# Optimization experiments

Measured on AMD Instinct MI355X. Metric: run time of the kernel, lower is better.

Reference implementation:

```python
import jax, jax.numpy as jnp
import numpy as np

E, H = 1024, 16
N, S, T = 2, 2048, 2048


def setup_inputs() -> dict:
    key = jax.random.key(0)
    ks = jax.random.split(key, 8)
    scale = 1.0 / np.sqrt(E)
    q = jax.random.normal(ks[0], (N, S, E), dtype=jnp.float32)
    k = jax.random.normal(ks[1], (N, T, E), dtype=jnp.float32)
    v = jax.random.normal(ks[2], (N, T, E), dtype=jnp.float32)
    pad_mask = jax.random.randint(ks[3], (N, 1, 1, T), 0, 2, dtype=jnp.int32)
    subsq_mask = jnp.tril(jnp.ones((S, T), dtype=jnp.int32))[None, None]
    Wq = jax.random.normal(ks[4], (E, E), dtype=jnp.float32) * scale
    Wk = jax.random.normal(ks[5], (E, E), dtype=jnp.float32) * scale
    Wv = jax.random.normal(ks[6], (E, E), dtype=jnp.float32) * scale
    bq = jnp.zeros((E,), dtype=jnp.float32)
    bk = jnp.zeros((E,), dtype=jnp.float32)
    bv = jnp.zeros((E,), dtype=jnp.float32)
    return {"query": q, "key": k, "value": v, "pad_mask": pad_mask,
            "subsq_mask": subsq_mask, "Wq": Wq, "bq": bq, "Wk": Wk,
            "bk": bk, "Wv": Wv, "bv": bv}


def reference(query, key, value, pad_mask, subsq_mask, Wq, bq, Wk, bk, Wv, bv):
    n, s, e = query.shape
    t = value.shape[1]
    d = e // H
    # Linear projections (torch Linear: x @ W^T + b), split into heads
    q = (query @ Wq.T + bq).reshape(n, s, H, d).transpose(0, 2, 1, 3)  # [N,H,S,D]
    k = (key @ Wk.T + bk).reshape(n, t, H, d).transpose(0, 2, 1, 3)    # [N,H,T,D]
    v = (value @ Wv.T + bv).reshape(n, t, H, d).transpose(0, 2, 1, 3)  # [N,H,T,D]
    att = jnp.einsum('bhsd,bhtd->bhst', q, k) / jnp.sqrt(jnp.float32(d))
    att = jnp.where(pad_mask == 0, jnp.float32(-1e9), att)
    att = jnp.where(subsq_mask == 0, jnp.float32(-1e9), att)
    prob = jax.nn.softmax(att, axis=-1)
    out = jnp.einsum('bhst,bhtd->bhsd', prob, v)  # [N,H,S,D]
    return out.transpose(0, 2, 1, 3).reshape(n, s, e)
```

## Files before the change

kernel.cpp:

```cpp
#include <hip/hip_runtime.h>

#define HEADS 16
#define DH    64
#define EMB   1024
#define NBAT  2
#define SEQ   2048
#define KDIM  1024
#define NROW  (NBAT * SEQ)

typedef __attribute__((ext_vector_type(8))) short short8;
typedef __attribute__((ext_vector_type(4))) short short4v;
typedef __attribute__((ext_vector_type(4))) float floatx4;
typedef unsigned short u16;
typedef unsigned int   u32;
typedef unsigned long long u64;

__device__ __forceinline__ u16 f2bf(float x) {
    u32 u = __builtin_bit_cast(u32, x);
    u += 0x7fffu + ((u >> 16) & 1u);
    return (u16)(u >> 16);
}
__device__ __forceinline__ float bf2f(u16 v) {
    return __builtin_bit_cast(float, ((u32)v) << 16);
}

__device__ __forceinline__ void gll16(const u16* g, u16* l) {
    __builtin_amdgcn_global_load_lds((const __attribute__((address_space(1))) u32*)g,
                                     (__attribute__((address_space(3))) u32*)l, 16, 0, 0);
}

__global__ __launch_bounds__(256) void cvt_kernel(
    const float* __restrict__ q, const float* __restrict__ k, const float* __restrict__ v,
    const float* __restrict__ wq, const float* __restrict__ wk, const float* __restrict__ wv,
    u16* __restrict__ xb, u16* __restrict__ wb)
{
    const int z = blockIdx.y;
    const float* src; u16* dst; int n;
    if (z < 3) { src = (z == 0) ? q : (z == 1) ? k : v;     dst = xb + (size_t)z * 4194304;       n = 4194304; }
    else       { src = (z == 3) ? wq : (z == 4) ? wk : wv;  dst = wb + (size_t)(z - 3) * 1048576; n = 1048576; }
    for (int i = (blockIdx.x * 256 + threadIdx.x) * 8; i < n; i += 512 * 256 * 8) {
        float4 a = *(const float4*)(src + i);
        float4 b = *(const float4*)(src + i + 4);
        short8 o;
        o[0] = (short)f2bf(a.x); o[1] = (short)f2bf(a.y); o[2] = (short)f2bf(a.z); o[3] = (short)f2bf(a.w);
        o[4] = (short)f2bf(b.x); o[5] = (short)f2bf(b.y); o[6] = (short)f2bf(b.z); o[7] = (short)f2bf(b.w);
        *(short8*)(dst + i) = o;
    }
}

__global__ __launch_bounds__(256) void proj_kernel(
    const u16* __restrict__ xb, const u16* __restrict__ wb,
    const float* __restrict__ bq, const float* __restrict__ bk, const float* __restrict__ bv,
    u16* __restrict__ qh, u16* __restrict__ kh, u16* __restrict__ vt)
{
    const int f = blockIdx.x;
    const int xcd = f & 7, jj = f >> 3;
    const int g  = xcd * 12 + (jj >> 3);
    const int nx = jj & 7;
    const int z  = g >> 5, y = g & 31;

    const u16* A  = xb + (size_t)z * 4194304;
    const u16* B  = wb + (size_t)z * 1048576;
    const float* Bp = (z == 0) ? bq : (z == 1) ? bk : bv;
    u16* dst        = (z == 0) ? qh : (z == 1) ? kh : vt;

    const int m0 = y * 128;
    const int n0 = nx * 128;
    const int tid  = threadIdx.x;
    const int wave = tid >> 6, lane = tid & 63;
    const int quad = lane >> 4, l15 = lane & 15;
    const int waveM = wave >> 1, waveN = wave & 1;
    const int sw = l15 & 7;

    __shared__ __align__(16) u16 smem[2 * 128 * 64];
    u16* As = smem;
    u16* Bs = smem + 128 * 64;

    floatx4 acc[4][4];
    for (int a = 0; a < 4; a++)
        for (int b = 0; b < 4; b++)
            acc[a][b] = floatx4{0.f, 0.f, 0.f, 0.f};

    const int lrow = lane >> 3;
    const int gcol = ((lane & 7) ^ lrow) * 8;

    for (int k0 = 0; k0 < KDIM; k0 += 64) {
        for (int j = 0; j < 4; j++) {
            int r8 = wave * 32 + j * 8;
            gll16(A + (size_t)(m0 + r8 + lrow) * KDIM + k0 + gcol, &As[r8 * 64]);
        }
        for (int j = 0; j < 4; j++) {
            int r8 = wave * 32 + j * 8;
            gll16(B + (size_t)(n0 + r8 + lrow) * KDIM + k0 + gcol, &Bs[r8 * 64]);
        }
        __syncthreads();

        for (int ks = 0; ks < 2; ks++) {
            short8 af[4], bfg[4];
            for (int mb = 0; mb < 4; mb++)
                af[mb]  = *(const short8*)&As[(waveM * 64 + mb * 16 + l15) * 64 + ((ks * 4 + quad) ^ sw) * 8];
            for (int nb = 0; nb < 4; nb++)
                bfg[nb] = *(const short8*)&Bs[(waveN * 64 + nb * 16 + l15) * 64 + ((ks * 4 + quad) ^ sw) * 8];
            for (int mb = 0; mb < 4; mb++)
                for (int nb = 0; nb < 4; nb++)
                    acc[mb][nb] = __builtin_amdgcn_mfma_f32_16x16x32_bf16(af[mb], bfg[nb], acc[mb][nb], 0, 0, 0);
        }
        __syncthreads();
    }

    if (z != 2) {
        const int row0 = m0 + waveM * 64;
        const int col0 = n0 + waveN * 64;
        const float scale = (z == 0) ? 0.125f * 1.44269504f : 1.0f;
        for (int nb = 0; nb < 4; nb++) {
            int col = col0 + nb * 16 + l15;
            float bias = Bp[col];
            int hh = col >> 6, dd = col & 63;
            for (int mb = 0; mb < 4; mb++) {
                for (int r = 0; r < 4; r++) {
                    int row = row0 + mb * 16 + quad * 4 + r;
                    int nn = row >> 11, ss = row & 2047;
                    dst[((size_t)(nn * HEADS + hh) * SEQ + ss) * DH + dd] =
                        f2bf((acc[mb][nb][r] + bias) * scale);
                }
            }
        }
    } else {
        const int nn  = m0 >> 11;
        const int ss0 = m0 & 2047;
        for (int p = 0; p < 2; p++) {
            if (waveN == p) {
                for (int nb = 0; nb < 4; nb++) {
                    int col_l = nb * 16 + l15;
                    float bias = Bp[n0 + p * 64 + col_l];
                    for (int mb = 0; mb < 4; mb++) {
                        short4v pk;
                        for (int r = 0; r < 4; r++)
                            pk[r] = (short)f2bf(acc[mb][nb][r] + bias);
                        *(short4v*)&smem[col_l * 136 + waveM * 64 + mb * 16 + quad * 4] = pk;
                    }
                }
            }
            __syncthreads();
            const int hh = (n0 >> 6) + p;
            u16* drow = dst + ((size_t)(nn * HEADS + hh) * DH) * SEQ + ss0;
            for (int c2 = tid; c2 < 1024; c2 += 256) {
                int dl = c2 >> 4, tc = (c2 & 15) * 8;
                short8 vv = *(const short8*)&smem[dl * 136 + tc];
                *(short8*)(drow + (size_t)dl * SEQ + tc) = vv;
            }
            __syncthreads();
        }
    }
}

__global__ __launch_bounds__(256) void vmean_kernel(const u16* __restrict__ vt,
                                                    float* __restrict__ vmean)
{
    const int row = blockIdx.x;
    const u16* p = vt + (size_t)row * SEQ;
    const int tid = threadIdx.x;
    float s = 0.f;
    for (int i = tid; i < SEQ; i += 256) s += bf2f(p[i]);
    __shared__ float red[256];
    red[tid] = s;
    __syncthreads();
    for (int st = 128; st > 0; st >>= 1) {
        if (tid < st) red[tid] += red[tid + st];
        __syncthreads();
    }
    if (tid == 0) vmean[row] = red[0] * (1.f / (float)SEQ);
}

__global__ __launch_bounds__(256) void attn_kernel(
    const u16* __restrict__ qh, const u16* __restrict__ kh, const u16* __restrict__ vt,
    const int* __restrict__ pad, const float* __restrict__ vmean,
    float* __restrict__ out)
{
    const int f = blockIdx.x;
    const int xcd = f & 7, jj = f >> 3;
    const int nh = xcd * 4 + (jj >> 4);
    const int pr = jj & 15;
    const int n = nh >> 4, h = nh & 15;
    const int tid  = threadIdx.x;
    const int wave = tid >> 6, lane = tid & 63;
    const int quad = lane >> 4, l15 = lane & 15;
    const int sw = l15 & 7;

    __shared__ __align__(16) u16 Ks[2][64 * 64];
    __shared__ __align__(16) u16 Vs[2][64 * 64];
    __shared__ __align__(16) u16 Ps[64 * 72];
    __shared__ u64 padb[32];

    {
        const int* pp = pad + n * SEQ;
        for (int i = 0; i < 8; i++) {
            int seg = wave * 8 + i;
            u64 m = __ballot(pp[seg * 64 + lane] != 0);
            if (lane == 0) padb[seg] = m;
        }
    }

    const u16* qbase = qh + (size_t)nh * SEQ * DH;
    const u16* kbase = kh + (size_t)nh * SEQ * DH;
    const u16* vbase = vt + (size_t)nh * DH * SEQ;

    short8 ones;
    for (int i = 0; i < 8; i++) ones[i] = (short)0x3F80;
    float vm[4];
    for (int nd = 0; nd < 4; nd++) vm[nd] = vmean[nh * DH + nd * 16 + l15];

    const int lrow = lane >> 3;
    const int gcol = ((lane & 7) ^ lrow) * 8;

    for (int half = 0; half < 2; half++) {
        const int sb = half ? (31 - pr) : pr;
        const int s0 = sb * 64;
        const int nt = sb + 1;
        const int srow = s0 + wave * 16 + l15;

        short8 qf[2];
        for (int ks = 0; ks < 2; ks++)
            qf[ks] = *(const short8*)(qbase + (size_t)srow * DH + ks * 32 + quad * 8);

        floatx4 oacc[4], lacc;
        for (int nd = 0; nd < 4; nd++) oacc[nd] = floatx4{0.f, 0.f, 0.f, 0.f};
        lacc = floatx4{0.f, 0.f, 0.f, 0.f};

        __syncthreads();

        for (int j = 0; j < 2; j++) {
            int r8 = wave * 16 + j * 8;
            gll16(kbase + (size_t)(r8 + lrow) * DH + gcol, &Ks[0][r8 * 64]);
            gll16(vbase + (size_t)(r8 + lrow) * SEQ + gcol, &Vs[0][r8 * 64]);
        }

        for (int tb = 0; tb < nt; tb++) {
            const int cur = tb & 1;
            __syncthreads();

            if (tb + 1 < nt) {
                const int t0n = (tb + 1) * 64;
                for (int j = 0; j < 2; j++) {
                    int r8 = wave * 16 + j * 8;
                    gll16(kbase + (size_t)(t0n + r8 + lrow) * DH + gcol, &Ks[1 - cur][r8 * 64]);
                    gll16(vbase + (size_t)(r8 + lrow) * SEQ + t0n + gcol, &Vs[1 - cur][r8 * 64]);
                }
            }

            const int t0 = tb * 64;
            const u64 w = padb[t0 >> 6];
            const bool diag = (tb == sb);

            floatx4 sc[4];
            for (int nb = 0; nb < 4; nb++) sc[nb] = floatx4{0.f, 0.f, 0.f, 0.f};
            __builtin_amdgcn_s_setprio(1);
            for (int ks = 0; ks < 2; ks++)
                for (int nb = 0; nb < 4; nb++) {
                    short8 kf = *(const short8*)&Ks[cur][(nb * 16 + l15) * 64 + ((ks * 4 + quad) ^ sw) * 8];
                    sc[nb] = __builtin_amdgcn_mfma_f32_16x16x32_bf16(kf, qf[ks], sc[nb], 0, 0, 0);
                }
            __builtin_amdgcn_s_setprio(0);

            for (int nb = 0; nb < 4; nb++) {
                short4v pk;
                for (int r = 0; r < 4; r++) {
                    int sh = nb * 16 + quad * 4 + r;
                    bool ok = ((w >> sh) & 1ull) != 0;
                    if (diag) ok = ok && (t0 + sh <= srow);
                    float p = ok ? __builtin_amdgcn_exp2f(sc[nb][r]) : 0.f;
                    pk[r] = (short)f2bf(p);
                }
                *(short4v*)&Ps[(wave * 16 + l15) * 72 + nb * 16 + quad * 4] = pk;
            }
            asm volatile("s_waitcnt lgkmcnt(0)" ::: "memory");

            __builtin_amdgcn_s_setprio(1);
            for (int ks = 0; ks < 2; ks++) {
                short8 pa = *(const short8*)&Ps[(wave * 16 + l15) * 72 + ks * 32 + quad * 8];
                for (int nd = 0; nd < 4; nd++) {
                    short8 vb = *(const short8*)&Vs[cur][(nd * 16 + l15) * 64 + ((ks * 4 + quad) ^ sw) * 8];
                    oacc[nd] = __builtin_amdgcn_mfma_f32_16x16x32_bf16(pa, vb, oacc[nd], 0, 0, 0);
                }
                lacc = __builtin_amdgcn_mfma_f32_16x16x32_bf16(pa, ones, lacc, 0, 0, 0);
            }
            __builtin_amdgcn_s_setprio(0);
        }

        for (int r = 0; r < 4; r++) {
            float l = lacc[r];
            int s = s0 + wave * 16 + quad * 4 + r;
            float* orow = out + (size_t)(n * SEQ + s) * EMB + h * DH;
            if (l > 0.f) {
                float inv = 1.f / l;
                for (int nd = 0; nd < 4; nd++) orow[nd * 16 + l15] = oacc[nd][r] * inv;
            } else {
                for (int nd = 0; nd < 4; nd++) orow[nd * 16 + l15] = vm[nd];
            }
        }
    }
}

extern "C" void kernel_launch(void* const* d_in, const int* in_sizes, int n_in,
                              void* d_out, int out_size, void* d_ws, size_t ws_size,
                              hipStream_t stream)
{
    const float* qin = (const float*)d_in[0];
    const float* kin = (const float*)d_in[1];
    const float* vin = (const float*)d_in[2];
    const int*   pad = (const int*)d_in[3];
    const float* Wq = (const float*)d_in[5];
    const float* bq = (const float*)d_in[6];
    const float* Wk = (const float*)d_in[7];
    const float* bk = (const float*)d_in[8];
    const float* Wv = (const float*)d_in[9];
    const float* bv = (const float*)d_in[10];
    float* out = (float*)d_out;

    const size_t per = (size_t)NBAT * HEADS * SEQ * DH;
    u16* qh = (u16*)d_ws;
    u16* kh = qh + per;
    u16* vt = kh + per;
    float* vmean = (float*)(vt + per);
    u16* xb = (u16*)(vmean + 2048);
    u16* wb = xb + 3 * per;

    cvt_kernel<<<dim3(512, 6), 256, 0, stream>>>(qin, kin, vin, Wq, Wk, Wv, xb, wb);
    proj_kernel<<<dim3(768), 256, 0, stream>>>(xb, wb, bq, bk, bv, qh, kh, vt);
    vmean_kernel<<<dim3(NBAT * HEADS * DH), 256, 0, stream>>>(vt, vmean);
    attn_kernel<<<dim3(512), 256, 0, stream>>>(qh, kh, vt, pad, vmean, out);
}
```

Baseline: 219.3 us.

## Process paired causal query blocks jointly to share K/V tile loads

Each block used to process its two query tiles (pr and 31-pr) one after the other, loading K/V twice for the shared prefix. Now both tiles are processed together over the common prefix, with each K/V tile loaded once and fed to both score and PV MFMAs, and the later tail then continues for the longer tile alone. Block index to pair mapping is also interleaved so neighbouring blocks get balanced pairs. This halves K/V LDS traffic and syncs over the prefix, at the cost of more registers (two accumulator sets) and a larger P buffer in LDS, which may reduce occupancy.

Measured after the change: 229.5 us. +4.6%, slower.

```diff
diff --git a/kernel.cpp b/kernel.cpp
--- a/kernel.cpp
+++ b/kernel.cpp
@@ -180,7 +180,8 @@
     const int f = blockIdx.x;
     const int xcd = f & 7, jj = f >> 3;
     const int nh = xcd * 4 + (jj >> 4);
-    const int pr = jj & 15;
+    const int idx = jj & 15;
+    const int pr = (idx & 1) ? (15 - (idx >> 1)) : (idx >> 1);
     const int n = nh >> 4, h = nh & 15;
     const int tid  = threadIdx.x;
     const int wave = tid >> 6, lane = tid & 63;
@@ -189,7 +190,7 @@
 
     __shared__ __align__(16) u16 Ks[2][64 * 64];
     __shared__ __align__(16) u16 Vs[2][64 * 64];
-    __shared__ __align__(16) u16 Ps[64 * 72];
+    __shared__ __align__(16) u16 Ps[128 * 72];
     __shared__ u64 padb[32];
 
     {
@@ -213,90 +214,170 @@
     const int lrow = lane >> 3;
     const int gcol = ((lane & 7) ^ lrow) * 8;
 
-    for (int half = 0; half < 2; half++) {
-        const int sb = half ? (31 - pr) : pr;
-        const int s0 = sb * 64;
-        const int nt = sb + 1;
-        const int srow = s0 + wave * 16 + l15;
-
-        short8 qf[2];
+    const int sbA = pr, sbB = 31 - pr;
+    const int s0A = sbA * 64, s0B = sbB * 64;
+    const int srowA = s0A + wave * 16 + l15;
+    const int srowB = s0B + wave * 16 + l15;
+    const int prow = (wave * 16 + l15) * 72;
+
+    short8 qfA[2], qfB[2];
+    for (int ks = 0; ks < 2; ks++) {
+        qfA[ks] = *(const short8*)(qbase + (size_t)srowA * DH + ks * 32 + quad * 8);
+        qfB[ks] = *(const short8*)(qbase + (size_t)srowB * DH + ks * 32 + quad * 8);
+    }
+
+    floatx4 oaccA[4], laccA, oaccB[4], laccB;
+    for (int nd = 0; nd < 4; nd++) {
+        oaccA[nd] = floatx4{0.f, 0.f, 0.f, 0.f};
+        oaccB[nd] = floatx4{0.f, 0.f, 0.f, 0.f};
+    }
+    laccA = floatx4{0.f, 0.f, 0.f, 0.f};
+    laccB = floatx4{0.f, 0.f, 0.f, 0.f};
+
+    __syncthreads();
+
+    for (int j2 = 0; j2 < 2; j2++) {
+        int r8 = wave * 16 + j2 * 8;
+        gll16(kbase + (size_t)(r8 + lrow) * DH + gcol, &Ks[0][r8 * 64]);
+        gll16(vbase + (size_t)(r8 + lrow) * SEQ + gcol, &Vs[0][r8 * 64]);
+    }
+
+    for (int tb = 0; tb <= sbA; tb++) {
+        const int cur = tb & 1;
+        __syncthreads();
+
+        {
+            const int t0n = (tb + 1) * 64;
+            for (int j2 = 0; j2 < 2; j2++) {
+                int r8 = wave * 16 + j2 * 8;
+                gll16(kbase + (size_t)(t0n + r8 + lrow) * DH + gcol, &Ks[1 - cur][r8 * 64]);
+                gll16(vbase + (size_t)(r8 + lrow) * SEQ + t0n + gcol, &Vs[1 - cur][r8 * 64]);
+            }
+        }
+
+        const int t0 = tb * 64;
+        const u64 w = padb[tb];
+        const bool diagA = (tb == sbA);
+
+        floatx4 scA[4], scB[4];
+        for (int nb = 0; nb < 4; nb++) {
+            scA[nb] = floatx4{0.f, 0.f, 0.f, 0.f};
+            scB[nb] = floatx4{0.f, 0.f, 0.f, 0.f};
+        }
+        __builtin_amdgcn_s_setprio(1);
         for (int ks = 0; ks < 2; ks++)
-            qf[ks] = *(const short8*)(qbase + (size_t)srow * DH + ks * 32 + quad * 8);
-
-        floatx4 oacc[4], lacc;
-        for (int nd = 0; nd < 4; nd++) oacc[nd] = floatx4{0.f, 0.f, 0.f, 0.f};
-        lacc = floatx4{0.f, 0.f, 0.f, 0.f};
-
+            for (int nb = 0; nb < 4; nb++) {
+                short8 kf = *(const short8*)&Ks[cur][(nb * 16 + l15) * 64 + ((ks * 4 + quad) ^ sw) * 8];
+                scA[nb] = __builtin_amdgcn_mfma_f32_16x16x32_bf16(kf, qfA[ks], scA[nb], 0, 0, 0);
+                scB[nb] = __builtin_amdgcn_mfma_f32_16x16x32_bf16(kf, qfB[ks], scB[nb], 0, 0, 0);
+            }
+        __builtin_amdgcn_s_setprio(0);
+
+        for (int nb = 0; nb < 4; nb++) {
+            const int shb = nb * 16 + quad * 4;
+            u32 wq = (u32)(w >> shb) & 0xFu;
+            short4v pkA, pkB;
+            for (int r = 0; r < 4; r++) {
+                bool okb = ((wq >> r) & 1u) != 0;
+                bool okA = okb && (!diagA || (t0 + shb + r <= srowA));
+                float pA_ = okA ? __builtin_amdgcn_exp2f(scA[nb][r]) : 0.f;
+                float pB_ = okb ? __builtin_amdgcn_exp2f(scB[nb][r]) : 0.f;
+                pkA[r] = (short)f2bf(pA_);
+                pkB[r] = (short)f2bf(pB_);
+            }
+            *(short4v*)&Ps[prow + shb] = pkA;
+            *(short4v*)&Ps[64 * 72 + prow + shb] = pkB;
+        }
+        asm volatile("s_waitcnt lgkmcnt(0)" ::: "memory");
+
+        __builtin_amdgcn_s_setprio(1);
+        for (int ks = 0; ks < 2; ks++) {
+            short8 paA = *(const short8*)&Ps[prow + ks * 32 + quad * 8];
+            short8 paB = *(const short8*)&Ps[64 * 72 + prow + ks * 32 + quad * 8];
+            for (int nd = 0; nd < 4; nd++) {
+                short8 vb = *(const short8*)&Vs[cur][(nd * 16 + l15) * 64 + ((ks * 4 + quad) ^ sw) * 8];
+                oaccA[nd] = __builtin_amdgcn_mfma_f32_16x16x32_bf16(paA, vb, oaccA[nd], 0, 0, 0);
+                oaccB[nd] = __builtin_amdgcn_mfma_f32_16x16x32_bf16(paB, vb, oaccB[nd], 0, 0, 0);
+            }
+            laccA = __builtin_amdgcn_mfma_f32_16x16x32_bf16(paA, ones, laccA, 0, 0, 0);
+            laccB = __builtin_amdgcn_mfma_f32_16x16x32_bf16(paB, ones, laccB, 0, 0, 0);
+        }
+        __builtin_amdgcn_s_setprio(0);
+    }
+
+    for (int tb = sbA + 1; tb <= sbB; tb++) {
+        const int cur = tb & 1;
         __syncthreads();
 
-        for (int j = 0; j < 2; j++) {
-            int r8 = wave * 16 + j * 8;
-            gll16(kbase + (size_t)(r8 + lrow) * DH + gcol, &Ks[0][r8 * 64]);
-            gll16(vbase + (size_t)(r8 + lrow) * SEQ + gcol, &Vs[0][r8 * 64]);
-        }
-
-        for (int tb = 0; tb < nt; tb++) {
-            const int cur = tb & 1;
-            __syncthreads();
-
-            if (tb + 1 < nt) {
-                const int t0n = (tb + 1) * 64;
-                for (int j = 0; j < 2; j++) {
-                    int r8 = wave * 16 + j * 8;
-                    gll16(kbase + (size_t)(t0n + r8 + lrow) * DH + gcol, &Ks[1 - cur][r8 * 64]);
-                    gll16(vbase + (size_t)(r8 + lrow) * SEQ + t0n + gcol, &Vs[1 - cur][r8 * 64]);
-                }
-            }
-
-            const int t0 = tb * 64;
-            const u64 w = padb[t0 >> 6];
-            const bool diag = (tb == sb);
-
-            floatx4 sc[4];
-            for (int nb = 0; nb < 4; nb++) sc[nb] = floatx4{0.f, 0.f, 0.f, 0.f};
-            __builtin_amdgcn_s_setprio(1);
-            for (int ks = 0; ks < 2; ks++)
-                for (int nb = 0; nb < 4; nb++) {
-                    short8 kf = *(const short8*)&Ks[cur][(nb * 16 + l15) * 64 + ((ks * 4 + quad) ^ sw) * 8];
-                    sc[nb] = __builtin_amdgcn_mfma_f32_16x16x32_bf16(kf, qf[ks], sc[nb], 0, 0, 0);
-                }
-            __builtin_amdgcn_s_setprio(0);
-
+        if (tb + 1 <= sbB) {
+            const int t0n = (tb + 1) * 64;
+            for (int j2 = 0; j2 < 2; j2++) {
+                int r8 = wave * 16 + j2 * 8;
+                gll16(kbase + (size_t)(t0n + r8 + lrow) * DH + gcol, &Ks[1 - cur][r8 * 64]);
+                gll16(vbase + (size_t)(r8 + lrow) * SEQ + t0n + gcol, &Vs[1 - cur][r8 * 64]);
+            }
+        }
+
+        const int t0 = tb * 64;
+        const u64 w = padb[tb];
+        const bool diagB = (tb == sbB);
+
+        floatx4 scB[4];
+        for (int nb = 0; nb < 4; nb++) scB[nb] = floatx4{0.f, 0.f, 0.f, 0.f};
+        __builtin_amdgcn_s_setprio(1);
+        for (int ks = 0; ks < 2; ks++)
             for (int nb = 0; nb < 4; nb++) {
-                short4v pk;
-                for (int r = 0; r < 4; r++) {
-                    int sh = nb * 16 + quad * 4 + r;
-                    bool ok = ((w >> sh) & 1ull) != 0;
-                    if (diag) ok = ok && (t0 + sh <= srow);
-                    float p = ok ? __builtin_amdgcn_exp2f(sc[nb][r]) : 0.f;
-                    pk[r] = (short)f2bf(p);
-                }
-                *(short4v*)&Ps[(wave * 16 + l15) * 72 + nb * 16 + quad * 4] = pk;
-            }
-            asm volatile("s_waitcnt lgkmcnt(0)" ::: "memory");
-
-            __builtin_amdgcn_s_setprio(1);
-            for (int ks = 0; ks < 2; ks++) {
-                short8 pa = *(const short8*)&Ps[(wave * 16 + l15) * 72 + ks * 32 + quad * 8];
-                for (int nd = 0; nd < 4; nd++) {
-                    short8 vb = *(const short8*)&Vs[cur][(nd * 16 + l15) * 64 + ((ks * 4 + quad) ^ sw) * 8];
-                    oacc[nd] = __builtin_amdgcn_mfma_f32_16x16x32_bf16(pa, vb, oacc[nd], 0, 0, 0);
-                }
-                lacc = __builtin_amdgcn_mfma_f32_16x16x32_bf16(pa, ones, lacc, 0, 0, 0);
-            }
-            __builtin_amdgcn_s_setprio(0);
-        }
-
-        for (int r = 0; r < 4; r++) {
-            float l = lacc[r];
-            int s = s0 + wave * 16 + quad * 4 + r;
-            float* orow = out + (size_t)(n * SEQ + s) * EMB + h * DH;
-            if (l > 0.f) {
-                float inv = 1.f / l;
-                for (int nd = 0; nd < 4; nd++) orow[nd * 16 + l15] = oacc[nd][r] * inv;
-            } else {
-                for (int nd = 0; nd < 4; nd++) orow[nd * 16 + l15] = vm[nd];
-            }
+                short8 kf = *(const short8*)&Ks[cur][(nb * 16 + l15) * 64 + ((ks * 4 + quad) ^ sw) * 8];
+                scB[nb] = __builtin_amdgcn_mfma_f32_16x16x32_bf16(kf, qfB[ks], scB[nb], 0, 0, 0);
+            }
+        __builtin_amdgcn_s_setprio(0);
+
+        for (int nb = 0; nb < 4; nb++) {
+            const int shb = nb * 16 + quad * 4;
+            u32 wq = (u32)(w >> shb) & 0xFu;
+            short4v pkB;
+            for (int r = 0; r < 4; r++) {
+                bool okb = ((wq >> r) & 1u) != 0;
+                if (diagB) okb = okb && (t0 + shb + r <= srowB);
+                float pB_ = okb ? __builtin_amdgcn_exp2f(scB[nb][r]) : 0.f;
+                pkB[r] = (short)f2bf(pB_);
+            }
+            *(short4v*)&Ps[64 * 72 + prow + shb] = pkB;
+        }
+        asm volatile("s_waitcnt lgkmcnt(0)" ::: "memory");
+
+        __builtin_amdgcn_s_setprio(1);
+        for (int ks = 0; ks < 2; ks++) {
+            short8 paB = *(const short8*)&Ps[64 * 72 + prow + ks * 32 + quad * 8];
+            for (int nd = 0; nd < 4; nd++) {
+                short8 vb = *(const short8*)&Vs[cur][(nd * 16 + l15) * 64 + ((ks * 4 + quad) ^ sw) * 8];
+                oaccB[nd] = __builtin_amdgcn_mfma_f32_16x16x32_bf16(paB, vb, oaccB[nd], 0, 0, 0);
+            }
+            laccB = __builtin_amdgcn_mfma_f32_16x16x32_bf16(paB, ones, laccB, 0, 0, 0);
+        }
+        __builtin_amdgcn_s_setprio(0);
+    }
+
+    for (int r = 0; r < 4; r++) {
+        float l = laccA[r];
+        int s = s0A + wave * 16 + quad * 4 + r;
+        float* orow = out + (size_t)(n * SEQ + s) * EMB + h * DH;
+        if (l > 0.f) {
+            float inv = 1.f / l;
+            for (int nd = 0; nd < 4; nd++) orow[nd * 16 + l15] = oaccA[nd][r] * inv;
+        } else {
+            for (int nd = 0; nd < 4; nd++) orow[nd * 16 + l15] = vm[nd];
+        }
+    }
+    for (int r = 0; r < 4; r++) {
+        float l = laccB[r];
+        int s = s0B + wave * 16 + quad * 4 + r;
+        float* orow = out + (size_t)(n * SEQ + s) * EMB + h * DH;
+        if (l > 0.f) {
+            float inv = 1.f / l;
+            for (int nd = 0; nd < 4; nd++) orow[nd * 16 + l15] = oaccB[nd][r] * inv;
+        } else {
+            for (int nd = 0; nd < 4; nd++) orow[nd * 16 + l15] = vm[nd];
         }
     }
 }
```
